# Kernel tuning notes

Hardware: AMD Instinct MI355X
Metric: run time of the kernel (lower is better)

## Reference

```python
import jax, jax.numpy as jnp
import numpy as np

N = 65536
IN_DIM = 512
H1, H2 = 256, 128
LATENT = 3
SINDY_DIM = 22  # latent=3, poly_order=3: 3 ones + 3 linear + 6 quad + 10 cubic


def _mlp(v, w0, b0, w1, b1, w2, b2):
    # Linear+Sigmoid, Linear+Sigmoid, Linear+Identity (matches encoder/decoder stacks)
    h = jax.nn.sigmoid(v @ w0 + b0)
    h = jax.nn.sigmoid(h @ w1 + b1)
    return h @ w2 + b2


def _sindy_library(z):
    # Faithful to sindy_library(): d ones columns, then linear, quad (i<=j), cubic (i<=j<=k)
    n, d = z.shape
    cols = [jnp.ones((n,), z.dtype) for _ in range(d)]
    cols += [z[:, i] for i in range(d)]
    for i in range(d):
        for j in range(i, d):
            cols.append(z[:, i] * z[:, j])
    for i in range(d):
        for j in range(i, d):
            for k in range(j, d):
                cols.append(z[:, i] * z[:, j] * z[:, k])
    return jnp.stack(cols, axis=1)


def _mean_jac(fn, x):
    # torch: jacobian of batched fn, take block-diagonal (per-sample Jacobians), mean over samples
    return jax.vmap(jax.jacrev(fn))(x).mean(axis=0)


def setup_inputs():
    key = jax.random.key(0)
    ks = jax.random.split(key, 12)

    def glorot(k, i, o):
        return jax.random.normal(k, (i, o), jnp.float32) * np.float32(np.sqrt(2.0 / (i + o)))

    return {
        "x": jax.random.normal(ks[0], (N, IN_DIM), jnp.float32),
        "dx": jax.random.normal(ks[1], (N, IN_DIM), jnp.float32),
        "ddx": jax.random.normal(ks[2], (N, IN_DIM), jnp.float32),
        "enc_w0": glorot(ks[3], IN_DIM, H1), "enc_b0": jnp.zeros((H1,), jnp.float32),
        "enc_w1": glorot(ks[4], H1, H2), "enc_b1": jnp.zeros((H2,), jnp.float32),
        "enc_w2": glorot(ks[5], H2, LATENT), "enc_b2": jnp.zeros((LATENT,), jnp.float32),
        "dec_w0": glorot(ks[6], LATENT, H2), "dec_b0": jnp.zeros((H2,), jnp.float32),
        "dec_w1": glorot(ks[7], H2, H1), "dec_b1": jnp.zeros((H1,), jnp.float32),
        "dec_w2": glorot(ks[8], H1, IN_DIM), "dec_b2": jnp.zeros((IN_DIM,), jnp.float32),
        "E_w": jnp.ones((SINDY_DIM, LATENT), jnp.float32),  # nn.init.ones_ on E.weight
        "E_b": jnp.zeros((LATENT,), jnp.float32),
    }


def reference(x, dx, ddx, enc_w0, enc_b0, enc_w1, enc_b1, enc_w2, enc_b2,
              dec_w0, dec_b0, dec_w1, dec_b1, dec_w2, dec_b2, E_w, E_b):
    enc = lambda v: _mlp(v, enc_w0, enc_b0, enc_w1, enc_b1, enc_w2, enc_b2)
    dec = lambda v: _mlp(v, dec_w0, dec_b0, dec_w1, dec_b1, dec_w2, dec_b2)

    z = enc(x)                      # [N, LATENT]
    Je = _mean_jac(enc, x)          # [LATENT, IN_DIM]  batch-mean encoder Jacobian
    dz = dx @ Je.T                  # [N, LATENT]
    theta = _sindy_library(z)       # [N, SINDY_DIM]
    dzb = theta @ E_w + E_b         # [N, LATENT]  SINDy prediction E(theta)
    xb = dec(z)                     # [N, IN_DIM]
    Jd = _mean_jac(dec, z)          # [IN_DIM, LATENT]  batch-mean decoder Jacobian
    dxb = dzb @ Jd.T                # [N, IN_DIM]
    return (z, dz, dzb, xb, dxb)
```

## Files before the change

### kernel.cpp

```cpp
#include <hip/hip_runtime.h>

#define NROWS 65536
#define COVAR_Z 256

typedef unsigned short u16;
typedef short bf16x8 __attribute__((ext_vector_type(8)));
typedef u16 u16x8 __attribute__((ext_vector_type(8)));
typedef float f32x4 __attribute__((ext_vector_type(4)));

__device__ __forceinline__ u16 f2bf(float f) {
  unsigned int u = __builtin_bit_cast(unsigned int, f);
  u += 0x7FFFu + ((u >> 16) & 1u);
  return (u16)(u >> 16);
}
__device__ __forceinline__ float bf2f(u16 s) {
  return __builtin_bit_cast(float, (unsigned int)s << 16);
}
__device__ __forceinline__ float sigd(u16 s) {
  const float p = bf2f(s);
  return p * (1.0f - p);
}

__global__ void prep_weights(const float* __restrict__ eW0, const float* __restrict__ eW1,
                             const float* __restrict__ dW1, const float* __restrict__ dW2,
                             u16* __restrict__ eW0t, u16* __restrict__ eW1t,
                             u16* __restrict__ dW1t, u16* __restrict__ dW2t) {
  const int idx = blockIdx.x * 256 + threadIdx.x;
  if (idx < 131072) {
    const int n = idx >> 9, k = idx & 511;
    eW0t[idx] = f2bf(eW0[k * 256 + n]);
  } else if (idx < 163840) {
    const int j = idx - 131072, n = j >> 8, k = j & 255;
    eW1t[j] = f2bf(eW1[k * 128 + n]);
  } else if (idx < 196608) {
    const int j = idx - 163840, n = j >> 7, k = j & 127;
    dW1t[j] = f2bf(dW1[k * 256 + n]);
  } else {
    const int j = idx - 196608, n = j >> 8, k = j & 255;
    dW2t[j] = f2bf(dW2[k * 512 + n]);
  }
}

template <int ACT, int A_F32>
__global__ __launch_bounds__(256, 2) void gemm_mfma(const void* __restrict__ Av,
                                                    const u16* __restrict__ Wt,
                                                    const float* __restrict__ bias,
                                                    void* __restrict__ Cv, int K, int Nc) {
  __shared__ u16 As[128 * 32];
  __shared__ u16 Bs[128 * 32];
  const int tid = threadIdx.x;
  const int lane = tid & 63;
  const int wave = tid >> 6;

  const int gx = gridDim.x;
  const int nwg = gx * gridDim.y;
  int id = blockIdx.y * gx + blockIdx.x;
  id = (id & 7) * (nwg >> 3) + (id >> 3);
  const int lgx = __builtin_ctz(gx);
  const int n0 = (id & (gx - 1)) * 128;
  const int m0 = (id >> lgx) * 128;

  const int wm = (wave & 1) * 64;
  const int wn = (wave >> 1) * 64;
  const int q = lane >> 4;
  const int mr = lane & 15;

  f32x4 acc[4][4] = {};

  for (int k0 = 0; k0 < K; k0 += 32) {
    if (A_F32) {
      const float* A = (const float*)Av;
#pragma unroll
      for (int i = 0; i < 2; ++i) {
        const int c = tid + i * 256;
        const int r = c >> 2, p = c & 3;
        const int g = (p - (r >> 1)) & 3;
        const float* src = A + (size_t)(m0 + r) * K + k0 + g * 8;
        const float4 v0 = *(const float4*)src;
        const float4 v1 = *(const float4*)(src + 4);
        u16x8 w;
        w[0] = f2bf(v0.x); w[1] = f2bf(v0.y); w[2] = f2bf(v0.z); w[3] = f2bf(v0.w);
        w[4] = f2bf(v1.x); w[5] = f2bf(v1.y); w[6] = f2bf(v1.z); w[7] = f2bf(v1.w);
        *(u16x8*)&As[c * 8] = w;
      }
    } else {
      const u16* A = (const u16*)Av;
#pragma unroll
      for (int i = 0; i < 2; ++i) {
        const int c = tid + i * 256;
        const int r = c >> 2, p = c & 3;
        const int g = (p - (r >> 1)) & 3;
        __builtin_amdgcn_global_load_lds(
            (const __attribute__((address_space(1))) void*)(A + (size_t)(m0 + r) * K + k0 + g * 8),
            (__attribute__((address_space(3))) void*)&As[(i * 256 + wave * 64) * 8], 16, 0, 0);
      }
    }
    {
#pragma unroll
      for (int i = 0; i < 2; ++i) {
        const int c = tid + i * 256;
        const int r = c >> 2, p = c & 3;
        const int g = (p - (r >> 1)) & 3;
        __builtin_amdgcn_global_load_lds(
            (const __attribute__((address_space(1))) void*)(Wt + (size_t)(n0 + r) * K + k0 + g * 8),
            (__attribute__((address_space(3))) void*)&Bs[(i * 256 + wave * 64) * 8], 16, 0, 0);
      }
    }
    __syncthreads();

    bf16x8 af[4], bfr[4];
#pragma unroll
    for (int i = 0; i < 4; ++i) {
      const int r = wm + i * 16 + mr;
      const int col = (q + (r >> 1)) & 3;
      af[i] = *(const bf16x8*)&As[r * 32 + col * 8];
    }
#pragma unroll
    for (int j = 0; j < 4; ++j) {
      const int r = wn + j * 16 + mr;
      const int col = (q + (r >> 1)) & 3;
      bfr[j] = *(const bf16x8*)&Bs[r * 32 + col * 8];
    }
#pragma unroll
    for (int i = 0; i < 4; ++i)
#pragma unroll
      for (int j = 0; j < 4; ++j)
        acc[i][j] = __builtin_amdgcn_mfma_f32_16x16x32_bf16(af[i], bfr[j], acc[i][j], 0, 0, 0);
    __syncthreads();
  }

  const int orow = (lane >> 4) * 4;
  const int ocol = lane & 15;
#pragma unroll
  for (int j = 0; j < 4; ++j) {
    const int col = n0 + wn + j * 16 + ocol;
    const float bj = bias[col];
#pragma unroll
    for (int i = 0; i < 4; ++i) {
      const int rbase = m0 + wm + i * 16 + orow;
#pragma unroll
      for (int r = 0; r < 4; ++r) {
        float v = acc[i][j][r] + bj;
        if (ACT) {
          v = 1.0f / (1.0f + __expf(-v));
          ((u16*)Cv)[(size_t)(rbase + r) * Nc + col] = f2bf(v);
        } else {
          ((float*)Cv)[(size_t)(rbase + r) * Nc + col] = v;
        }
      }
    }
  }
}

__global__ __launch_bounds__(256, 2) void covar128(const u16* __restrict__ P,
                                                   const u16* __restrict__ Q,
                                                   float* __restrict__ partial,
                                                   int Ap, int Bq, int chunk) {
  __shared__ float Ps[16][132];
  __shared__ float Qs[16][132];
  const int tid = threadIdx.x;

  const int gx = gridDim.x, gy = gridDim.y;
  const int nwg = gx * gy * gridDim.z;
  int id = (blockIdx.z * gy + blockIdx.y) * gx + blockIdx.x;
  id = (id & 7) * (nwg >> 3) + (id >> 3);
  const int lgx = __builtin_ctz(gx), lgy = __builtin_ctz(gy);
  const int bx = id & (gx - 1);
  const int by = (id >> lgx) & (gy - 1);
  const int bz = id >> (lgx + lgy);

  const int a0 = bx * 128;
  const int b0 = by * 128;
  const int nbase = bz * chunk;
  const int tx = tid & 15, ty = tid >> 4;
  float acc[8][8] = {};

  for (int nn = 0; nn < chunk; nn += 16) {
    {
      const u16* pr = P + (size_t)(nbase + nn + ty) * Ap + a0;
      const ushort4 v0 = *(const ushort4*)(pr + tx * 4);
      const ushort4 v1 = *(const ushort4*)(pr + 64 + tx * 4);
      float4 f0, f1;
      f0.x = sigd(v0.x); f0.y = sigd(v0.y); f0.z = sigd(v0.z); f0.w = sigd(v0.w);
      f1.x = sigd(v1.x); f1.y = sigd(v1.y); f1.z = sigd(v1.z); f1.w = sigd(v1.w);
      *(float4*)&Ps[ty][tx * 4] = f0;
      *(float4*)&Ps[ty][64 + tx * 4] = f1;
    }
    {
      const u16* qr = Q + (size_t)(nbase + nn + ty) * Bq + b0;
      const ushort4 v0 = *(const ushort4*)(qr + tx * 4);
      const ushort4 v1 = *(const ushort4*)(qr + 64 + tx * 4);
      float4 f0, f1;
      f0.x = sigd(v0.x); f0.y = sigd(v0.y); f0.z = sigd(v0.z); f0.w = sigd(v0.w);
      f1.x = sigd(v1.x); f1.y = sigd(v1.y); f1.z = sigd(v1.z); f1.w = sigd(v1.w);
      *(float4*)&Qs[ty][tx * 4] = f0;
      *(float4*)&Qs[ty][64 + tx * 4] = f1;
    }
    __syncthreads();
#pragma unroll
    for (int kk = 0; kk < 16; ++kk) {
      float av[8], bv[8];
      *(float4*)&av[0] = *(const float4*)&Ps[kk][ty * 4];
      *(float4*)&av[4] = *(const float4*)&Ps[kk][64 + ty * 4];
      *(float4*)&bv[0] = *(const float4*)&Qs[kk][tx * 4];
      *(float4*)&bv[4] = *(const float4*)&Qs[kk][64 + tx * 4];
#pragma unroll
      for (int i = 0; i < 8; ++i)
#pragma unroll
        for (int j = 0; j < 8; ++j) acc[i][j] += av[i] * bv[j];
    }
    __syncthreads();
  }

  float* outp = partial + (size_t)bz * Ap * Bq;
#pragma unroll
  for (int i = 0; i < 8; ++i) {
    const int ar = (i < 4) ? (ty * 4 + i) : (64 + ty * 4 + (i - 4));
    float4 v0, v1;
    v0.x = acc[i][0]; v0.y = acc[i][1]; v0.z = acc[i][2]; v0.w = acc[i][3];
    v1.x = acc[i][4]; v1.y = acc[i][5]; v1.z = acc[i][6]; v1.w = acc[i][7];
    *(float4*)&outp[(size_t)(a0 + ar) * Bq + b0 + tx * 4] = v0;
    *(float4*)&outp[(size_t)(a0 + ar) * Bq + b0 + 64 + tx * 4] = v1;
  }
}

__global__ void reduce_partial(const float* __restrict__ partial, float* __restrict__ out,
                               int S, int Z) {
  const int i = blockIdx.x * 256 + threadIdx.x;
  float s = 0.f;
  for (int z = 0; z < Z; ++z) s += partial[(size_t)z * S + i];
  out[i] = s;
}

__global__ void enc_l3_sindy(const u16* __restrict__ h2, const float* __restrict__ W2,
                             const float* __restrict__ b2, const float* __restrict__ Ew,
                             const float* __restrict__ Eb, float* __restrict__ z_out,
                             float* __restrict__ dzb_out) {
  const int lane = threadIdx.x & 63;
  const int row = blockIdx.x * 4 + (threadIdx.x >> 6);
  const ushort2 h = *(const ushort2*)(h2 + (size_t)row * 128 + lane * 2);
  const float hx = bf2f(h.x), hy = bf2f(h.y);
  const int k = lane * 2;
  float s[3];
#pragma unroll
  for (int l = 0; l < 3; ++l)
    s[l] = hx * W2[k * 3 + l] + hy * W2[(k + 1) * 3 + l];
#pragma unroll
  for (int off = 32; off > 0; off >>= 1) {
    s[0] += __shfl_xor(s[0], off);
    s[1] += __shfl_xor(s[1], off);
    s[2] += __shfl_xor(s[2], off);
  }
  if (lane == 0) {
    const float z0 = s[0] + b2[0];
    const float z1 = s[1] + b2[1];
    const float z2 = s[2] + b2[2];
    z_out[row * 3 + 0] = z0;
    z_out[row * 3 + 1] = z1;
    z_out[row * 3 + 2] = z2;
    float th[22];
    th[0] = 1.f; th[1] = 1.f; th[2] = 1.f;
    th[3] = z0; th[4] = z1; th[5] = z2;
    th[6] = z0 * z0; th[7] = z0 * z1; th[8] = z0 * z2;
    th[9] = z1 * z1; th[10] = z1 * z2; th[11] = z2 * z2;
    th[12] = z0 * z0 * z0; th[13] = z0 * z0 * z1; th[14] = z0 * z0 * z2;
    th[15] = z0 * z1 * z1; th[16] = z0 * z1 * z2; th[17] = z0 * z2 * z2;
    th[18] = z1 * z1 * z1; th[19] = z1 * z1 * z2; th[20] = z1 * z2 * z2;
    th[21] = z2 * z2 * z2;
    float d0 = Eb[0], d1 = Eb[1], d2 = Eb[2];
#pragma unroll
    for (int c = 0; c < 22; ++c) {
      d0 += th[c] * Ew[c * 3 + 0];
      d1 += th[c] * Ew[c * 3 + 1];
      d2 += th[c] * Ew[c * 3 + 2];
    }
    dzb_out[row * 3 + 0] = d0;
    dzb_out[row * 3 + 1] = d1;
    dzb_out[row * 3 + 2] = d2;
  }
}

__global__ void t1je_kernel(const float* __restrict__ Ce, const float* __restrict__ W2,
                            const float* __restrict__ W1, const float* __restrict__ W0,
                            float* __restrict__ Je) {
  __shared__ float T1s[768];
  const int t = threadIdx.x;
  {
    const int b = t & 255, l = t >> 8;
    float acc = 0.f;
    for (int a = 0; a < 128; ++a)
      acc += W2[a * 3 + l] * W1[b * 128 + a] * Ce[a * 256 + b];
    T1s[l * 256 + b] = acc * (1.0f / 65536.0f);
  }
  __syncthreads();
  for (int idx = t; idx < 1536; idx += 768) {
    const int l = idx >> 9, k = idx & 511;
    const float* t1r = &T1s[l * 256];
    float acc = 0.f;
    for (int b = 0; b < 256; ++b) acc += t1r[b] * W0[(size_t)k * 256 + b];
    Je[l * 512 + k] = acc;
  }
}

__global__ void t2jd_kernel(const float* __restrict__ Cd, const float* __restrict__ V1,
                            const float* __restrict__ V0, const float* __restrict__ V2,
                            float* __restrict__ Jd) {
  __shared__ float T2s[768];
  const int t = threadIdx.x;
  {
    const int a = t & 255, l = t >> 8;
    float acc = 0.f;
    for (int b = 0; b < 128; ++b)
      acc += Cd[a * 128 + b] * V1[b * 256 + a] * V0[l * 128 + b];
    T2s[a * 3 + l] = acc * (1.0f / 65536.0f);
  }
  __syncthreads();
  for (int idx = t; idx < 1536; idx += 768) {
    const int k = idx & 511, l = idx >> 9;
    float acc = 0.f;
    for (int a = 0; a < 256; ++a) acc += V2[(size_t)a * 512 + k] * T2s[a * 3 + l];
    Jd[k * 3 + l] = acc;
  }
}

__global__ void dz_kernel(const float* __restrict__ dx, const float* __restrict__ Je,
                          float* __restrict__ dz) {
  __shared__ float sJe[1536];
  for (int i = threadIdx.x; i < 1536; i += 256) sJe[i] = Je[i];
  __syncthreads();
  const int lane = threadIdx.x & 63;
  const int row = blockIdx.x * 4 + (threadIdx.x >> 6);
  const int k = lane * 8;
  const float4 v0 = *(const float4*)(dx + (size_t)row * 512 + k);
  const float4 v1 = *(const float4*)(dx + (size_t)row * 512 + k + 4);
  float s[3];
#pragma unroll
  for (int l = 0; l < 3; ++l) {
    const float* j = sJe + l * 512 + k;
    s[l] = v0.x * j[0] + v0.y * j[1] + v0.z * j[2] + v0.w * j[3] +
           v1.x * j[4] + v1.y * j[5] + v1.z * j[6] + v1.w * j[7];
  }
#pragma unroll
  for (int off = 32; off > 0; off >>= 1) {
    s[0] += __shfl_xor(s[0], off);
    s[1] += __shfl_xor(s[1], off);
    s[2] += __shfl_xor(s[2], off);
  }
  if (lane == 0) {
    dz[row * 3 + 0] = s[0];
    dz[row * 3 + 1] = s[1];
    dz[row * 3 + 2] = s[2];
  }
}

__global__ void dec_l1(const float* __restrict__ z, const float* __restrict__ V0,
                       const float* __restrict__ b0, u16* __restrict__ h1d) {
  const int t = threadIdx.x;
  const int j0 = (t & 15) * 8;
  const int n = blockIdx.x * 16 + (t >> 4);
  float w0[8], w1[8], w2[8], bb[8];
  *(float4*)&w0[0] = *(const float4*)(V0 + j0);
  *(float4*)&w0[4] = *(const float4*)(V0 + j0 + 4);
  *(float4*)&w1[0] = *(const float4*)(V0 + 128 + j0);
  *(float4*)&w1[4] = *(const float4*)(V0 + 128 + j0 + 4);
  *(float4*)&w2[0] = *(const float4*)(V0 + 256 + j0);
  *(float4*)&w2[4] = *(const float4*)(V0 + 256 + j0 + 4);
  *(float4*)&bb[0] = *(const float4*)(b0 + j0);
  *(float4*)&bb[4] = *(const float4*)(b0 + j0 + 4);
  const float z0 = z[n * 3 + 0], z1 = z[n * 3 + 1], z2 = z[n * 3 + 2];
  u16x8 o;
#pragma unroll
  for (int m = 0; m < 8; ++m) {
    const float v = z0 * w0[m] + z1 * w1[m] + z2 * w2[m] + bb[m];
    o[m] = f2bf(1.0f / (1.0f + __expf(-v)));
  }
  *(u16x8*)(h1d + (size_t)n * 128 + j0) = o;
}

__global__ void dxb_kernel(const float* __restrict__ dzb, const float* __restrict__ Jd,
                           float* __restrict__ dxb) {
  const int t = threadIdx.x;
  const int k0 = (t & 63) * 8;
  const int rbase = blockIdx.x * 16 + (t >> 6);
  float jf[24];
#pragma unroll
  for (int q = 0; q < 6; ++q)
    *(float4*)&jf[q * 4] = *(const float4*)(Jd + k0 * 3 + q * 4);
#pragma unroll
  for (int it = 0; it < 4; ++it) {
    const int n = rbase + it * 4;
    const float d0 = dzb[n * 3 + 0], d1 = dzb[n * 3 + 1], d2 = dzb[n * 3 + 2];
    float v[8];
#pragma unroll
    for (int m = 0; m < 8; ++m)
      v[m] = d0 * jf[m * 3 + 0] + d1 * jf[m * 3 + 1] + d2 * jf[m * 3 + 2];
    float* outp = dxb + (size_t)n * 512 + k0;
    *(float4*)&outp[0] = *(float4*)&v[0];
    *(float4*)&outp[4] = *(float4*)&v[4];
  }
}

extern "C" void kernel_launch(void* const* d_in, const int* in_sizes, int n_in,
                              void* d_out, int out_size, void* d_ws, size_t ws_size,
                              hipStream_t stream) {
  const int N = NROWS;
  const float* x   = (const float*)d_in[0];
  const float* dx  = (const float*)d_in[1];
  const float* eW0 = (const float*)d_in[3];
  const float* eb0 = (const float*)d_in[4];
  const float* eW1 = (const float*)d_in[5];
  const float* eb1 = (const float*)d_in[6];
  const float* eW2 = (const float*)d_in[7];
  const float* eb2 = (const float*)d_in[8];
  const float* dW0 = (const float*)d_in[9];
  const float* db0 = (const float*)d_in[10];
  const float* dW1 = (const float*)d_in[11];
  const float* db1 = (const float*)d_in[12];
  const float* dW2 = (const float*)d_in[13];
  const float* db2 = (const float*)d_in[14];
  const float* Ew  = (const float*)d_in[15];
  const float* Eb  = (const float*)d_in[16];

  float* out = (float*)d_out;
  float* z_out   = out;
  float* dz_out  = out + (size_t)N * 3;
  float* dzb_out = out + (size_t)N * 6;
  float* xb_out  = out + (size_t)N * 9;
  float* dxb_out = out + (size_t)N * 9 + (size_t)N * 512;

  u16* h1e = (u16*)d_ws;
  u16* h2e = h1e + (size_t)N * 256;
  u16* h2d = h1e;
  u16* h1d = h2e;
  u16* wbuf = h2e + (size_t)N * 128;
  u16* eW0t = wbuf;
  u16* eW1t = eW0t + 131072;
  u16* dW1t = eW1t + 32768;
  u16* dW2t = dW1t + 32768;
  float* partial = (float*)(dW2t + 131072);
  float* Ce = partial + (size_t)COVAR_Z * 32768;
  float* Cd = Ce + 32768;
  float* Je = Cd + 32768;
  float* Jd = Je + 1536;

  prep_weights<<<1280, 256, 0, stream>>>(eW0, eW1, dW1, dW2, eW0t, eW1t, dW1t, dW2t);

  gemm_mfma<1, 1><<<dim3(2, N / 128), 256, 0, stream>>>(x, eW0t, eb0, h1e, 512, 256);
  gemm_mfma<1, 0><<<dim3(1, N / 128), 256, 0, stream>>>(h1e, eW1t, eb1, h2e, 256, 128);
  enc_l3_sindy<<<N / 4, 256, 0, stream>>>(h2e, eW2, eb2, Ew, Eb, z_out, dzb_out);

  covar128<<<dim3(1, 2, COVAR_Z), 256, 0, stream>>>(h2e, h1e, partial, 128, 256, N / COVAR_Z);
  reduce_partial<<<128, 256, 0, stream>>>(partial, Ce, 32768, COVAR_Z);
  t1je_kernel<<<1, 768, 0, stream>>>(Ce, eW2, eW1, eW0, Je);
  dz_kernel<<<N / 4, 256, 0, stream>>>(dx, Je, dz_out);

  dec_l1<<<N / 16, 256, 0, stream>>>(z_out, dW0, db0, h1d);
  gemm_mfma<1, 0><<<dim3(2, N / 128), 256, 0, stream>>>(h1d, dW1t, db1, h2d, 128, 256);
  gemm_mfma<0, 0><<<dim3(4, N / 128), 256, 0, stream>>>(h2d, dW2t, db2, xb_out, 256, 512);

  covar128<<<dim3(2, 1, COVAR_Z), 256, 0, stream>>>(h2d, h1d, partial, 256, 128, N / COVAR_Z);
  reduce_partial<<<128, 256, 0, stream>>>(partial, Cd, 32768, COVAR_Z);
  t2jd_kernel<<<1, 768, 0, stream>>>(Cd, dW1, dW0, dW2, Jd);
  dxb_kernel<<<N / 16, 256, 0, stream>>>(dzb_out, Jd, dxb_out);
}
```

Before: 970.6 us.

## Move Jacobian covariance reductions onto bf16 MFMA with transposed sigmoid-derivative buffers

The GEMM and dec_l1 epilogues now also write the sigmoid derivative p(1-p) in bf16 into transposed (feature-major) buffers. The covariance kernels then run as bf16 MFMA GEMMs over the sample dimension, loading through global_load_lds, replacing the scalar fp32 FMA loops that recomputed derivatives from row-major activations. This trades extra transposed writes (scattered 8-byte stores) and a larger workspace for much cheaper covariance compute. Rounding the derivatives to bf16 adds some precision loss.

```diff
diff --git a/kernel.cpp b/kernel.cpp
--- a/kernel.cpp
+++ b/kernel.cpp
@@ -6,6 +6,7 @@
 typedef unsigned short u16;
 typedef short bf16x8 __attribute__((ext_vector_type(8)));
 typedef u16 u16x8 __attribute__((ext_vector_type(8)));
+typedef u16 u16x4 __attribute__((ext_vector_type(4)));
 typedef float f32x4 __attribute__((ext_vector_type(4)));
 
 __device__ __forceinline__ u16 f2bf(float f) {
@@ -15,10 +16,6 @@
 }
 __device__ __forceinline__ float bf2f(u16 s) {
   return __builtin_bit_cast(float, (unsigned int)s << 16);
-}
-__device__ __forceinline__ float sigd(u16 s) {
-  const float p = bf2f(s);
-  return p * (1.0f - p);
 }
 
 __global__ void prep_weights(const float* __restrict__ eW0, const float* __restrict__ eW1,
@@ -41,11 +38,13 @@
   }
 }
 
-template <int ACT, int A_F32>
+template <int ACT, int A_F32, int FT>
 __global__ __launch_bounds__(256, 2) void gemm_mfma(const void* __restrict__ Av,
                                                     const u16* __restrict__ Wt,
                                                     const float* __restrict__ bias,
-                                                    void* __restrict__ Cv, int K, int Nc) {
+                                                    void* __restrict__ Cv,
+                                                    u16* __restrict__ Ft,
+                                                    int K, int Nc) {
   __shared__ u16 As[128 * 32];
   __shared__ u16 Bs[128 * 32];
   const int tid = threadIdx.x;
@@ -138,27 +137,38 @@
 #pragma unroll
     for (int i = 0; i < 4; ++i) {
       const int rbase = m0 + wm + i * 16 + orow;
+      u16 fr[4];
 #pragma unroll
       for (int r = 0; r < 4; ++r) {
         float v = acc[i][j][r] + bj;
         if (ACT) {
           v = 1.0f / (1.0f + __expf(-v));
-          ((u16*)Cv)[(size_t)(rbase + r) * Nc + col] = f2bf(v);
+          const u16 sb = f2bf(v);
+          ((u16*)Cv)[(size_t)(rbase + r) * Nc + col] = sb;
+          if (FT) {
+            const float p = bf2f(sb);
+            fr[r] = f2bf(p * (1.0f - p));
+          }
         } else {
           ((float*)Cv)[(size_t)(rbase + r) * Nc + col] = v;
         }
       }
-    }
-  }
-}
-
-__global__ __launch_bounds__(256, 2) void covar128(const u16* __restrict__ P,
-                                                   const u16* __restrict__ Q,
-                                                   float* __restrict__ partial,
-                                                   int Ap, int Bq, int chunk) {
-  __shared__ float Ps[16][132];
-  __shared__ float Qs[16][132];
+      if (ACT && FT) {
+        *(u16x4*)&Ft[(size_t)col * NROWS + rbase] = *(u16x4*)&fr[0];
+      }
+    }
+  }
+}
+
+__global__ __launch_bounds__(256, 2) void covar_gemm(const u16* __restrict__ At,
+                                                     const u16* __restrict__ Bt,
+                                                     float* __restrict__ partial,
+                                                     int Ncb, int chunk) {
+  __shared__ u16 As[128 * 32];
+  __shared__ u16 Bs[128 * 32];
   const int tid = threadIdx.x;
+  const int lane = tid & 63;
+  const int wave = tid >> 6;
 
   const int gx = gridDim.x, gy = gridDim.y;
   const int nwg = gx * gy * gridDim.z;
@@ -169,58 +179,72 @@
   const int by = (id >> lgx) & (gy - 1);
   const int bz = id >> (lgx + lgy);
 
-  const int a0 = bx * 128;
-  const int b0 = by * 128;
-  const int nbase = bz * chunk;
-  const int tx = tid & 15, ty = tid >> 4;
-  float acc[8][8] = {};
-
-  for (int nn = 0; nn < chunk; nn += 16) {
-    {
-      const u16* pr = P + (size_t)(nbase + nn + ty) * Ap + a0;
-      const ushort4 v0 = *(const ushort4*)(pr + tx * 4);
-      const ushort4 v1 = *(const ushort4*)(pr + 64 + tx * 4);
-      float4 f0, f1;
-      f0.x = sigd(v0.x); f0.y = sigd(v0.y); f0.z = sigd(v0.z); f0.w = sigd(v0.w);
-      f1.x = sigd(v1.x); f1.y = sigd(v1.y); f1.z = sigd(v1.z); f1.w = sigd(v1.w);
-      *(float4*)&Ps[ty][tx * 4] = f0;
-      *(float4*)&Ps[ty][64 + tx * 4] = f1;
-    }
-    {
-      const u16* qr = Q + (size_t)(nbase + nn + ty) * Bq + b0;
-      const ushort4 v0 = *(const ushort4*)(qr + tx * 4);
-      const ushort4 v1 = *(const ushort4*)(qr + 64 + tx * 4);
-      float4 f0, f1;
-      f0.x = sigd(v0.x); f0.y = sigd(v0.y); f0.z = sigd(v0.z); f0.w = sigd(v0.w);
-      f1.x = sigd(v1.x); f1.y = sigd(v1.y); f1.z = sigd(v1.z); f1.w = sigd(v1.w);
-      *(float4*)&Qs[ty][tx * 4] = f0;
-      *(float4*)&Qs[ty][64 + tx * 4] = f1;
+  const int n0 = bx * 128;
+  const int m0 = by * 128;
+  const int kb = bz * chunk;
+
+  const int wm = (wave & 1) * 64;
+  const int wn = (wave >> 1) * 64;
+  const int q = lane >> 4;
+  const int mr = lane & 15;
+
+  f32x4 acc[4][4] = {};
+
+  for (int k0 = kb; k0 < kb + chunk; k0 += 32) {
+#pragma unroll
+    for (int i = 0; i < 2; ++i) {
+      const int c = tid + i * 256;
+      const int r = c >> 2, p = c & 3;
+      const int g = (p - (r >> 1)) & 3;
+      __builtin_amdgcn_global_load_lds(
+          (const __attribute__((address_space(1))) void*)(At + (size_t)(m0 + r) * NROWS + k0 + g * 8),
+          (__attribute__((address_space(3))) void*)&As[(i * 256 + wave * 64) * 8], 16, 0, 0);
+    }
+#pragma unroll
+    for (int i = 0; i < 2; ++i) {
+      const int c = tid + i * 256;
+      const int r = c >> 2, p = c & 3;
+      const int g = (p - (r >> 1)) & 3;
+      __builtin_amdgcn_global_load_lds(
+          (const __attribute__((address_space(1))) void*)(Bt + (size_t)(n0 + r) * NROWS + k0 + g * 8),
+          (__attribute__((address_space(3))) void*)&Bs[(i * 256 + wave * 64) * 8], 16, 0, 0);
     }
     __syncthreads();
-#pragma unroll
-    for (int kk = 0; kk < 16; ++kk) {
-      float av[8], bv[8];
-      *(float4*)&av[0] = *(const float4*)&Ps[kk][ty * 4];
-      *(float4*)&av[4] = *(const float4*)&Ps[kk][64 + ty * 4];
-      *(float4*)&bv[0] = *(const float4*)&Qs[kk][tx * 4];
-      *(float4*)&bv[4] = *(const float4*)&Qs[kk][64 + tx * 4];
-#pragma unroll
-      for (int i = 0; i < 8; ++i)
-#pragma unroll
-        for (int j = 0; j < 8; ++j) acc[i][j] += av[i] * bv[j];
-    }
+
+    bf16x8 af[4], bfr[4];
+#pragma unroll
+    for (int i = 0; i < 4; ++i) {
+      const int r = wm + i * 16 + mr;
+      const int col = (q + (r >> 1)) & 3;
+      af[i] = *(const bf16x8*)&As[r * 32 + col * 8];
+    }
+#pragma unroll
+    for (int j = 0; j < 4; ++j) {
+      const int r = wn + j * 16 + mr;
+      const int col = (q + (r >> 1)) & 3;
+      bfr[j] = *(const bf16x8*)&Bs[r * 32 + col * 8];
+    }
+#pragma unroll
+    for (int i = 0; i < 4; ++i)
+#pragma unroll
+      for (int j = 0; j < 4; ++j)
+        acc[i][j] = __builtin_amdgcn_mfma_f32_16x16x32_bf16(af[i], bfr[j], acc[i][j], 0, 0, 0);
     __syncthreads();
   }
 
-  float* outp = partial + (size_t)bz * Ap * Bq;
-#pragma unroll
-  for (int i = 0; i < 8; ++i) {
-    const int ar = (i < 4) ? (ty * 4 + i) : (64 + ty * 4 + (i - 4));
-    float4 v0, v1;
-    v0.x = acc[i][0]; v0.y = acc[i][1]; v0.z = acc[i][2]; v0.w = acc[i][3];
-    v1.x = acc[i][4]; v1.y = acc[i][5]; v1.z = acc[i][6]; v1.w = acc[i][7];
-    *(float4*)&outp[(size_t)(a0 + ar) * Bq + b0 + tx * 4] = v0;
-    *(float4*)&outp[(size_t)(a0 + ar) * Bq + b0 + 64 + tx * 4] = v1;
+  float* outp = partial + (size_t)bz * 32768;
+  const int orow = (lane >> 4) * 4;
+  const int ocol = lane & 15;
+#pragma unroll
+  for (int j = 0; j < 4; ++j) {
+    const int col = n0 + wn + j * 16 + ocol;
+#pragma unroll
+    for (int i = 0; i < 4; ++i) {
+      const int rbase = m0 + wm + i * 16 + orow;
+#pragma unroll
+      for (int r = 0; r < 4; ++r)
+        outp[(size_t)(rbase + r) * Ncb + col] = acc[i][j][r];
+    }
   }
 }
 
@@ -354,27 +378,26 @@
 }
 
 __global__ void dec_l1(const float* __restrict__ z, const float* __restrict__ V0,
-                       const float* __restrict__ b0, u16* __restrict__ h1d) {
+                       const float* __restrict__ b0, u16* __restrict__ h1d,
+                       u16* __restrict__ h1dT) {
   const int t = threadIdx.x;
-  const int j0 = (t & 15) * 8;
-  const int n = blockIdx.x * 16 + (t >> 4);
-  float w0[8], w1[8], w2[8], bb[8];
-  *(float4*)&w0[0] = *(const float4*)(V0 + j0);
-  *(float4*)&w0[4] = *(const float4*)(V0 + j0 + 4);
-  *(float4*)&w1[0] = *(const float4*)(V0 + 128 + j0);
-  *(float4*)&w1[4] = *(const float4*)(V0 + 128 + j0 + 4);
-  *(float4*)&w2[0] = *(const float4*)(V0 + 256 + j0);
-  *(float4*)&w2[4] = *(const float4*)(V0 + 256 + j0 + 4);
-  *(float4*)&bb[0] = *(const float4*)(b0 + j0);
-  *(float4*)&bb[4] = *(const float4*)(b0 + j0 + 4);
-  const float z0 = z[n * 3 + 0], z1 = z[n * 3 + 1], z2 = z[n * 3 + 2];
-  u16x8 o;
-#pragma unroll
-  for (int m = 0; m < 8; ++m) {
-    const float v = z0 * w0[m] + z1 * w1[m] + z2 * w2[m] + bb[m];
-    o[m] = f2bf(1.0f / (1.0f + __expf(-v)));
-  }
-  *(u16x8*)(h1d + (size_t)n * 128 + j0) = o;
+  const int j = t & 127;
+  const int half = t >> 7;
+  const int n0 = blockIdx.x * 32 + half * 16;
+  const float w0 = V0[j], w1 = V0[128 + j], w2 = V0[256 + j], bb = b0[j];
+  u16 fv[16];
+#pragma unroll
+  for (int s = 0; s < 16; ++s) {
+    const int n = n0 + s;
+    const float z0 = z[n * 3 + 0], z1 = z[n * 3 + 1], z2 = z[n * 3 + 2];
+    const float v = 1.0f / (1.0f + __expf(-(z0 * w0 + z1 * w1 + z2 * w2 + bb)));
+    const u16 sb = f2bf(v);
+    h1d[(size_t)n * 128 + j] = sb;
+    const float p = bf2f(sb);
+    fv[s] = f2bf(p * (1.0f - p));
+  }
+  *(u16x8*)&h1dT[(size_t)j * NROWS + n0] = *(u16x8*)&fv[0];
+  *(u16x8*)&h1dT[(size_t)j * NROWS + n0 + 8] = *(u16x8*)&fv[8];
 }
 
 __global__ void dxb_kernel(const float* __restrict__ dzb, const float* __restrict__ Jd,
@@ -428,11 +451,15 @@
   float* xb_out  = out + (size_t)N * 9;
   float* dxb_out = out + (size_t)N * 9 + (size_t)N * 512;
 
-  u16* h1e = (u16*)d_ws;
-  u16* h2e = h1e + (size_t)N * 256;
-  u16* h2d = h1e;
-  u16* h1d = h2e;
-  u16* wbuf = h2e + (size_t)N * 128;
+  u16* h1e  = (u16*)d_ws;
+  u16* h2e  = h1e  + (size_t)N * 256;
+  u16* h1eT = h2e  + (size_t)N * 128;
+  u16* h2eT = h1eT + (size_t)N * 256;
+  u16* h1d  = h2eT + (size_t)N * 128;
+  u16* h1dT = h1d  + (size_t)N * 128;
+  u16* h2d  = h1dT + (size_t)N * 128;
+  u16* h2dT = h2d  + (size_t)N * 256;
+  u16* wbuf = h2dT + (size_t)N * 256;
   u16* eW0t = wbuf;
   u16* eW1t = eW0t + 131072;
   u16* dW1t = eW1t + 32768;
@@ -443,22 +470,24 @@
   float* Je = Cd + 32768;
   float* Jd = Je + 1536;
 
+  const int chunk = N / COVAR_Z;
+
   prep_weights<<<1280, 256, 0, stream>>>(eW0, eW1, dW1, dW2, eW0t, eW1t, dW1t, dW2t);
 
-  gemm_mfma<1, 1><<<dim3(2, N / 128), 256, 0, stream>>>(x, eW0t, eb0, h1e, 512, 256);
-  gemm_mfma<1, 0><<<dim3(1, N / 128), 256, 0, stream>>>(h1e, eW1t, eb1, h2e, 256, 128);
+  gemm_mfma<1, 1, 1><<<dim3(2, N / 128), 256, 0, stream>>>(x, eW0t, eb0, h1e, h1eT, 512, 256);
+  gemm_mfma<1, 0, 1><<<dim3(1, N / 128), 256, 0, stream>>>(h1e, eW1t, eb1, h2e, h2eT, 256, 128);
   enc_l3_sindy<<<N / 4, 256, 0, stream>>>(h2e, eW2, eb2, Ew, Eb, z_out, dzb_out);
 
-  covar128<<<dim3(1, 2, COVAR_Z), 256, 0, stream>>>(h2e, h1e, partial, 128, 256, N / COVAR_Z);
+  covar_gemm<<<dim3(2, 1, COVAR_Z), 256, 0, stream>>>(h2eT, h1eT, partial, 256, chunk);
   reduce_partial<<<128, 256, 0, stream>>>(partial, Ce, 32768, COVAR_Z);
   t1je_kernel<<<1, 768, 0, stream>>>(Ce, eW2, eW1, eW0, Je);
   dz_kernel<<<N / 4, 256, 0, stream>>>(dx, Je, dz_out);
 
-  dec_l1<<<N / 16, 256, 0, stream>>>(z_out, dW0, db0, h1d);
-  gemm_mfma<1, 0><<<dim3(2, N / 128), 256, 0, stream>>>(h1d, dW1t, db1, h2d, 128, 256);
-  gemm_mfma<0, 0><<<dim3(4, N / 128), 256, 0, stream>>>(h2d, dW2t, db2, xb_out, 256, 512);
-
-  covar128<<<dim3(2, 1, COVAR_Z), 256, 0, stream>>>(h2d, h1d, partial, 256, 128, N / COVAR_Z);
+  dec_l1<<<N / 32, 256, 0, stream>>>(z_out, dW0, db0, h1d, h1dT);
+  gemm_mfma<1, 0, 1><<<dim3(2, N / 128), 256, 0, stream>>>(h1d, dW1t, db1, h2d, h2dT, 128, 256);
+  gemm_mfma<0, 0, 0><<<dim3(4, N / 128), 256, 0, stream>>>(h2d, dW2t, db2, xb_out, nullptr, 256, 512);
+
+  covar_gemm<<<dim3(1, 2, COVAR_Z), 256, 0, stream>>>(h2dT, h1dT, partial, 128, chunk);
   reduce_partial<<<128, 256, 0, stream>>>(partial, Cd, 32768, COVAR_Z);
   t2jd_kernel<<<1, 768, 0, stream>>>(Cd, dW1, dW0, dW2, Jd);
   dxb_kernel<<<N / 16, 256, 0, stream>>>(dzb_out, Jd, dxb_out);
```

After: 942.6 us. -2.9%, faster.
